# Kernel tuning notes

Hardware: AMD Instinct MI355X
Metric: run time of the kernel (lower is better)

## Reference

```python
import jax, jax.numpy as jnp
import numpy as np

N = 100000
E = 1600000
F_IN = 512
S_IN = 6
H = 64
C = 7


def gcn_conv(x, W, b, row, col, n):
    # PyG GCNConv: linear (no bias in lin), add self-loops, sym-normalize, scatter-add, + bias
    x = x @ W  # [N, out]
    loop = jnp.arange(n)
    r = jnp.concatenate([row, loop])
    c = jnp.concatenate([col, loop])
    deg = jax.ops.segment_sum(jnp.ones(r.shape, x.dtype), c, num_segments=n)
    dinv = jnp.where(deg > 0, deg ** -0.5, 0.0)
    norm = dinv[r] * dinv[c]  # [E+N]
    out = jax.ops.segment_sum(x[r] * norm[:, None], c, num_segments=n)
    return out + b


def setup_inputs() -> dict:
    key = jax.random.key(0)
    ks = jax.random.split(key, 12)
    feature = jax.random.normal(ks[0], (N, F_IN), jnp.float32)
    structure = jax.random.normal(ks[1], (N, S_IN), jnp.float32)
    edge_index = jax.random.randint(ks[2], (2, E), 0, N, dtype=jnp.int64)
    # glorot-ish param init
    def w(k, fan_in, fan_out):
        return jax.random.normal(k, (fan_in, fan_out), jnp.float32) * (1.0 / np.sqrt(fan_in))
    return {
        "feature": feature,
        "structure": structure,
        "edge_index": edge_index,
        "W_f": w(ks[3], F_IN, H), "b_f": jnp.zeros((H,), jnp.float32),
        "W_s": w(ks[4], S_IN, H), "b_s": jnp.zeros((H,), jnp.float32),
        "W_r": w(ks[5], 2 * H, C), "b_r": jnp.zeros((C,), jnp.float32),
        "emb": jax.random.normal(ks[6], (6, H), jnp.float32),
        "embW": jax.random.normal(ks[7], (H, 1), jnp.float32),
        "alpha_s": jnp.asarray(0.4, jnp.float32),
        "alpha_a": jnp.asarray(0.6, jnp.float32),
    }


def reference(feature, structure, edge_index, W_f, b_f, W_s, b_s, W_r, b_r, emb, embW, alpha_s, alpha_a):
    row, col = edge_index[0], edge_index[1]
    # branch 1: feature GCN (dropout is identity in eval mode)
    h_f = gcn_conv(feature, W_f, b_f, row, col, N)
    attr = h_f
    # embedding gate: sigmoid(emb @ embW) thresholded at 0.5 -> {0,1}
    gate = jax.nn.sigmoid(emb @ embW)  # [6,1]
    gate = jnp.where(gate < 0.5, 0.0, 1.0).astype(feature.dtype)
    struct_in = structure * gate[:, 0][None, :]  # [N,6] * [1,6]
    # branch 2: structure GCN
    h_s = gcn_conv(struct_in, W_s, b_s, row, col, N)
    struc = h_s
    # L1-normalize alphas (0.4,0.6 already sum to 1; torch does it via .data)
    denom = jax.lax.stop_gradient(jnp.abs(alpha_s) + jnp.abs(alpha_a))
    a_s = alpha_s / denom
    a_a = alpha_a / denom
    x = jnp.concatenate([attr * a_a * 2.0, struc * a_s * 2.0], axis=1)  # [N, 2H]
    y = gcn_conv(x, W_r, b_r, row, col, N)
    return (h_f, h_s, y)
```

## Files before the change

### kernel.cpp

```cpp
#include <hip/hip_runtime.h>
#include <hip/hip_bf16.h>


typedef __attribute__((ext_vector_type(8))) short bf16x8;
typedef __attribute__((ext_vector_type(4))) float f32x4;

__device__ __forceinline__ unsigned short f2bf(float x) {
    union { __hip_bfloat16 b; unsigned short u; } cv;
    cv.b = __float2bfloat16(x);
    return cv.u;
}
__device__ __forceinline__ float bf2f(unsigned short u) {
    union { unsigned u32; float f; } cv;
    cv.u32 = ((unsigned)u) << 16;
    return cv.f;
}

__global__ __launch_bounds__(256) void setup_prep_k(const float* __restrict__ emb,
                                                    const float* __restrict__ embW,
                                                    const float* __restrict__ alpha_s,
                                                    const float* __restrict__ alpha_a,
                                                    float* __restrict__ cw,
                                                    const float* __restrict__ Wf,
                                                    unsigned short* __restrict__ WthG,
                                                    unsigned short* __restrict__ WtlG,
                                                    unsigned* __restrict__ deg, int n) {
    if (blockIdx.x == 0) {
        if (threadIdx.x >= 64) return;
        int lane = threadIdx.x;
        float w = embW[lane];
        #pragma unroll
        for (int k = 0; k < 6; k++) {
            float p = emb[k * 64 + lane] * w;
            #pragma unroll
            for (int off = 32; off; off >>= 1) p += __shfl_xor(p, off);
            if (lane == 0) cw[k] = (p < 0.0f) ? 0.0f : 1.0f;
        }
        if (lane == 0) {
            float s = alpha_s[0];
            float a = alpha_a[0];
            float inv = 1.0f / (fabsf(s) + fabsf(a));
            cw[6] = 2.0f * a * inv;
            cw[7] = 2.0f * s * inv;
        }
        return;
    }
    if (blockIdx.x <= 128) {
        int idx = (blockIdx.x - 1) * 256 + threadIdx.x;
        int k = idx >> 6, c = idx & 63;
        float w = Wf[idx];
        unsigned short h = f2bf(w);
        unsigned short l = f2bf(w - bf2f(h));
        WthG[c * 512 + k] = h;
        WtlG[c * 512 + k] = l;
        return;
    }
    int start = (blockIdx.x - 129) * 1024 + threadIdx.x;
    #pragma unroll
    for (int k = 0; k < 4; k++) {
        int w = start + k * 256;
        if (w < n) deg[w] = 0u;
    }
}

__device__ __forceinline__ bool detect32(const int* p32, int e, int E, int lane) {
    int se = (e < E) ? e : lane;
    return __any(p32[2 * se + 1] != 0);
}

#define CHUNK 4096
__global__ __launch_bounds__(256) void degfill_k(const void* __restrict__ ei,
                                                 unsigned* __restrict__ deg,
                                                 int* __restrict__ slot, int E, int n) {
    int range = blockIdx.x & 7;
    int nper = (n + 7) >> 3;
    int lo = range * nper;
    int hi = min(n, lo + nper);
    int e0 = (blockIdx.x >> 3) * CHUNK + threadIdx.x;
    int lane = threadIdx.x & 63;
    const int* p32 = (const int*)ei;
    bool is32 = detect32(p32, e0, E, lane);

    int cs[16];
    #pragma unroll
    for (int k = 0; k < 16; k++) {
        int e = e0 + k * 256;
        cs[k] = -1;
        if (e < E)
            cs[k] = is32 ? p32[E + e] : (int)((const long long*)ei)[(size_t)E + e];
    }
    #pragma unroll
    for (int k = 0; k < 16; k++) {
        int c = cs[k];
        if (c < lo || c >= hi) continue;
        int e = e0 + k * 256;
        int r = is32 ? p32[e] : (int)((const long long*)ei)[(size_t)e];
        unsigned pos = atomicAdd(&deg[c], 1u);
        if (pos < 64u) slot[((size_t)c << 6) + pos] = r;
    }
}

__global__ void dinv_ss6_k(const unsigned* __restrict__ deg, float* __restrict__ dinv,
                           const float* __restrict__ structure, const float* __restrict__ cw,
                           unsigned short* __restrict__ ss6, int n) {
    int i = blockIdx.x * 256 + threadIdx.x;
    if (i >= n) return;
    float dv = rsqrtf((float)deg[i] + 1.0f);
    dinv[i] = dv;
    #pragma unroll
    for (int k = 0; k < 6; k++) ss6[i * 8 + k] = f2bf(structure[i * 6 + k] * cw[k] * dv);
    ss6[i * 8 + 6] = 0;
    ss6[i * 8 + 7] = 0;
}

__global__ __launch_bounds__(256) void gemm_f_mfma(const float* __restrict__ feat,
                                                   const unsigned short* __restrict__ WthG,
                                                   const unsigned short* __restrict__ WtlG,
                                                   const float* __restrict__ dinv,
                                                   unsigned short* __restrict__ xs, int n) {
    __shared__ unsigned short Ah[128 * 64];
    __shared__ unsigned short Bh[64 * 64];
    __shared__ unsigned short Bl[64 * 64];

    const int tid = threadIdx.x;
    const int blk = blockIdx.x;
    const int w = tid >> 6, l = tid & 63;
    const int lr = l & 15, lg = l >> 4;

    f32x4 acc[2][4];
    #pragma unroll
    for (int m = 0; m < 2; m++)
        #pragma unroll
        for (int nt = 0; nt < 4; nt++) acc[m][nt] = (f32x4)(0.0f);

    const int sr = tid >> 1, shalf = tid & 1;
    const int swc = tid >> 2, swq = tid & 3;
    const int gr_ld = min(blk * 128 + sr, n - 1);
    const float* asrc = feat + (size_t)gr_ld * 512 + shalf * 32;

    for (int k0 = 0; k0 < 512; k0 += 64) {
        {
            const float4* s4 = (const float4*)(asrc + k0);
            int base = sr * 128 + shalf * 64;
            int sw = (sr & 7) << 4;
            #pragma unroll
            for (int g = 0; g < 8; g++) {
                float4 v = s4[g];
                ushort4 h;
                h.x = f2bf(v.x); h.y = f2bf(v.y); h.z = f2bf(v.z); h.w = f2bf(v.w);
                *(ushort4*)((char*)Ah + ((base + g * 8) ^ sw)) = h;
            }
        }
        {
            int sw = (swc & 7) << 4;
            const unsigned short* wh = WthG + swc * 512 + k0;
            const unsigned short* wl = WtlG + swc * 512 + k0;
            #pragma unroll
            for (int s = 0; s < 2; s++) {
                int ko16 = swq * 2 + s;
                uint4 vh = *(const uint4*)(wh + ko16 * 8);
                uint4 vl = *(const uint4*)(wl + ko16 * 8);
                int off = (swc * 128 + ko16 * 16) ^ sw;
                *(uint4*)((char*)Bh + off) = vh;
                *(uint4*)((char*)Bl + off) = vl;
            }
        }
        __syncthreads();
        int swl = (lr & 7) << 4;
        #pragma unroll
        for (int ks = 0; ks < 2; ks++) {
            int koff = ks * 64 + lg * 16;
            int ra = ((w * 32 + lr) * 128 + koff) ^ swl;
            bf16x8 ah0 = *(const bf16x8*)((const char*)Ah + ra);
            bf16x8 ah1 = *(const bf16x8*)((const char*)Ah + ra + 16 * 128);
            #pragma unroll
            for (int nt = 0; nt < 4; nt++) {
                int cb = ((nt * 16 + lr) * 128 + koff) ^ swl;
                bf16x8 bh = *(const bf16x8*)((const char*)Bh + cb);
                bf16x8 bl = *(const bf16x8*)((const char*)Bl + cb);
                acc[0][nt] = __builtin_amdgcn_mfma_f32_16x16x32_bf16(ah0, bh, acc[0][nt], 0, 0, 0);
                acc[0][nt] = __builtin_amdgcn_mfma_f32_16x16x32_bf16(ah0, bl, acc[0][nt], 0, 0, 0);
                acc[1][nt] = __builtin_amdgcn_mfma_f32_16x16x32_bf16(ah1, bh, acc[1][nt], 0, 0, 0);
                acc[1][nt] = __builtin_amdgcn_mfma_f32_16x16x32_bf16(ah1, bl, acc[1][nt], 0, 0, 0);
            }
        }
        __syncthreads();
    }
    #pragma unroll
    for (int m = 0; m < 2; m++) {
        int row0 = blk * 128 + w * 32 + m * 16 + lg * 4;
        #pragma unroll
        for (int reg = 0; reg < 4; reg++) {
            int gr = row0 + reg;
            if (gr < n) {
                float dv = dinv[gr];
                #pragma unroll
                for (int nt = 0; nt < 4; nt++)
                    xs[(size_t)gr * 64 + nt * 16 + lr] = f2bf(acc[m][nt][reg] * dv);
            }
        }
    }
}

#define GATHER8(rl, g, accv, a6v)                                              \
    {                                                                          \
        int r0 = __shfl(rl, g + 0), r1 = __shfl(rl, g + 1);                    \
        int r2 = __shfl(rl, g + 2), r3 = __shfl(rl, g + 3);                    \
        int r4 = __shfl(rl, g + 4), r5 = __shfl(rl, g + 5);                    \
        int r6 = __shfl(rl, g + 6), r7 = __shfl(rl, g + 7);                    \
        float v0 = bf2f(xs[(size_t)r0 * 64 + lane]);                           \
        float v1 = bf2f(xs[(size_t)r1 * 64 + lane]);                           \
        float v2 = bf2f(xs[(size_t)r2 * 64 + lane]);                           \
        float v3 = bf2f(xs[(size_t)r3 * 64 + lane]);                           \
        float v4 = bf2f(xs[(size_t)r4 * 64 + lane]);                           \
        float v5 = bf2f(xs[(size_t)r5 * 64 + lane]);                           \
        float v6 = bf2f(xs[(size_t)r6 * 64 + lane]);                           \
        float v7 = bf2f(xs[(size_t)r7 * 64 + lane]);                           \
        accv += ((v0 + v1) + (v2 + v3)) + ((v4 + v5) + (v6 + v7));             \
        if (lane < 6) {                                                        \
            float u0 = bf2f(ss6[r0 * 8 + lane]), u1 = bf2f(ss6[r1 * 8 + lane]);\
            float u2 = bf2f(ss6[r2 * 8 + lane]), u3 = bf2f(ss6[r3 * 8 + lane]);\
            float u4 = bf2f(ss6[r4 * 8 + lane]), u5 = bf2f(ss6[r5 * 8 + lane]);\
            float u6 = bf2f(ss6[r6 * 8 + lane]), u7 = bf2f(ss6[r7 * 8 + lane]);\
            a6v += ((u0 + u1) + (u2 + u3)) + ((u4 + u5) + (u6 + u7));          \
        }                                                                      \
    }

__global__ __launch_bounds__(256) void agg_fs_k(const unsigned short* __restrict__ xs,
                                                const unsigned short* __restrict__ ss6,
                                                const int* __restrict__ slot,
                                                const unsigned* __restrict__ deg,
                                                const float* __restrict__ dinv,
                                                const float* __restrict__ cw,
                                                const float* __restrict__ bfv,
                                                const float* __restrict__ Ws,
                                                const float* __restrict__ bs,
                                                const float* __restrict__ Wr,
                                                float* __restrict__ out_hf,
                                                float* __restrict__ out_hs,
                                                unsigned short* __restrict__ ps, int n) {
    int wid = threadIdx.x >> 6;
    int lane = threadIdx.x & 63;
    int iA = blockIdx.x * 8 + wid * 2;
    int iB = iA + 1;
    if (iA >= n) return;
    bool hasB = iB < n;

    int dA = (int)min(deg[iA], 64u);
    int dB = hasB ? (int)min(deg[iB], 64u) : 0;

    float accA = bf2f(xs[(size_t)iA * 64 + lane]);
    float accB = hasB ? bf2f(xs[(size_t)iB * 64 + lane]) : 0.0f;
    float a6A = (lane < 6) ? bf2f(ss6[iA * 8 + lane]) : 0.0f;
    float a6B = (hasB && lane < 6) ? bf2f(ss6[iB * 8 + lane]) : 0.0f;

    int rlA = (lane < dA) ? slot[((size_t)iA << 6) + lane] : 0;
    int rlB = (lane < dB) ? slot[((size_t)iB << 6) + lane] : 0;
    int gmax = max(dA, dB);
    for (int g = 0; g + 8 <= gmax; g += 8) {
        if (g + 8 <= dA) GATHER8(rlA, g, accA, a6A);
        if (g + 8 <= dB) GATHER8(rlB, g, accB, a6B);
    }
    for (int d = dA & ~7; d < dA; d++) {
        int r = __shfl(rlA, d);
        accA += bf2f(xs[(size_t)r * 64 + lane]);
        if (lane < 6) a6A += bf2f(ss6[r * 8 + lane]);
    }
    for (int d = dB & ~7; d < dB; d++) {
        int r = __shfl(rlB, d);
        accB += bf2f(xs[(size_t)r * 64 + lane]);
        if (lane < 6) a6B += bf2f(ss6[r * 8 + lane]);
    }

    #pragma unroll
    for (int node = 0; node < 2; node++) {
        if (node == 1 && !hasB) break;
        int i = node ? iB : iA;
        float acc = node ? accB : accA;
        float a6 = node ? a6B : a6A;
        float di = dinv[i];
        float hf = acc * di + bfv[lane];
        float hs = bs[lane];
        #pragma unroll
        for (int k = 0; k < 6; k++) hs += __shfl(a6, k) * di * Ws[k * 64 + lane];
        out_hf[(size_t)i * 64 + lane] = hf;
        out_hs[(size_t)i * 64 + lane] = hs;

        float fa = hf * cw[6];
        float sa = hs * cw[7];
        #pragma unroll
        for (int j = 0; j < 7; j++) {
            float v = fa * Wr[lane * 7 + j] + sa * Wr[(64 + lane) * 7 + j];
            #pragma unroll
            for (int off = 32; off; off >>= 1) v += __shfl_xor(v, off);
            if (lane == j) ps[(size_t)i * 8 + j] = f2bf(v * di);
        }
        if (lane == 7) ps[(size_t)i * 8 + 7] = 0;
    }
}

__global__ __launch_bounds__(256) void agg_y_k(const unsigned short* __restrict__ ps,
                                               const int* __restrict__ slot,
                                               const unsigned* __restrict__ deg,
                                               const float* __restrict__ dinv,
                                               const float* __restrict__ br,
                                               float* __restrict__ out_y, int n) {
    int i = blockIdx.x * 4 + (threadIdx.x >> 6);
    int lane = threadIdx.x & 63;
    if (i >= n) return;
    int es = lane >> 3, j = lane & 7;
    int cnt = (int)min(deg[i], 64u);
    const int* srow = slot + ((size_t)i << 6);
    float acc = (es == 0) ? bf2f(ps[(size_t)i * 8 + j]) : 0.0f;
    int base = 0;
    for (; base + 16 <= cnt; base += 16) {
        int ra = srow[base + es];
        int rb = srow[base + 8 + es];
        acc += bf2f(ps[(size_t)ra * 8 + j]) + bf2f(ps[(size_t)rb * 8 + j]);
    }
    for (; base < cnt; base += 8) {
        int idx = base + es;
        if (idx < cnt) acc += bf2f(ps[(size_t)srow[idx] * 8 + j]);
    }
    acc += __shfl_xor(acc, 8);
    acc += __shfl_xor(acc, 16);
    acc += __shfl_xor(acc, 32);
    if (j < 7) out_y[(size_t)i * 7 + j] = acc * dinv[i] + br[j];
}

extern "C" void kernel_launch(void* const* d_in, const int* in_sizes, int n_in,
                              void* d_out, int out_size, void* d_ws, size_t ws_size,
                              hipStream_t stream) {
    const float* feature   = (const float*)d_in[0];
    const float* structure = (const float*)d_in[1];
    const void*  ei        = d_in[2];
    const float* Wf  = (const float*)d_in[3];
    const float* bfv = (const float*)d_in[4];
    const float* Ws  = (const float*)d_in[5];
    const float* bs  = (const float*)d_in[6];
    const float* Wr  = (const float*)d_in[7];
    const float* br  = (const float*)d_in[8];
    const float* emb = (const float*)d_in[9];
    const float* embW = (const float*)d_in[10];
    const float* alpha_s = (const float*)d_in[11];
    const float* alpha_a = (const float*)d_in[12];

    const int N = in_sizes[0] / 512;
    const int E = in_sizes[2] / 2;
    const int NB = (N + 255) / 256;
    const int NZ = (N + 1023) / 1024;
    const int NCH = (E + CHUNK - 1) / CHUNK;

    float* ws = (float*)d_ws;
    size_t XS     = 0;
    size_t SS6    = XS + (size_t)N * 32;
    size_t PS     = SS6 + (size_t)N * 4;
    size_t DINV   = PS + (size_t)N * 4;
    size_t DEG    = DINV + N;
    size_t CW     = DEG + N;
    size_t WT     = CW + 16;
    size_t SLOT   = WT + 32768;

    unsigned short* xs = (unsigned short*)(ws + XS);
    unsigned short* ss6 = (unsigned short*)(ws + SS6);
    unsigned short* ps = (unsigned short*)(ws + PS);
    float* dinv = ws + DINV;
    unsigned* deg = (unsigned*)(ws + DEG);
    float* cw = ws + CW;
    unsigned short* WthG = (unsigned short*)(ws + WT);
    unsigned short* WtlG = WthG + 512 * 64;
    int* slot = (int*)(ws + SLOT);

    setup_prep_k<<<129 + NZ, 256, 0, stream>>>(emb, embW, alpha_s, alpha_a, cw,
                                               Wf, WthG, WtlG, deg, N);
    degfill_k<<<NCH * 8, 256, 0, stream>>>(ei, deg, slot, E, N);
    dinv_ss6_k<<<NB, 256, 0, stream>>>(deg, dinv, structure, cw, ss6, N);
    gemm_f_mfma<<<(N + 127) / 128, 256, 0, stream>>>(feature, WthG, WtlG, dinv, xs, N);

    float* out_hf = (float*)d_out;
    float* out_hs = out_hf + (size_t)N * 64;
    float* out_y  = out_hf + (size_t)N * 128;
    agg_fs_k<<<(N + 7) / 8, 256, 0, stream>>>(xs, ss6, slot, deg, dinv, cw,
                                              bfv, Ws, bs, Wr, out_hf, out_hs, ps, N);
    agg_y_k<<<(N + 3) / 4, 256, 0, stream>>>(ps, slot, deg, dinv, br, out_y, N);
}
```

Before: 281.8 us.

## Load GEMM operands directly from global into registers, drop LDS staging

```diff
diff --git a/kernel.cpp b/kernel.cpp
--- a/kernel.cpp
+++ b/kernel.cpp
@@ -14,6 +14,14 @@
     union { unsigned u32; float f; } cv;
     cv.u32 = ((unsigned)u) << 16;
     return cv.f;
+}
+__device__ __forceinline__ bf16x8 cvt8(float4 a, float4 b) {
+    bf16x8 r;
+    r[0] = (short)f2bf(a.x); r[1] = (short)f2bf(a.y);
+    r[2] = (short)f2bf(a.z); r[3] = (short)f2bf(a.w);
+    r[4] = (short)f2bf(b.x); r[5] = (short)f2bf(b.y);
+    r[6] = (short)f2bf(b.z); r[7] = (short)f2bf(b.w);
+    return r;
 }
 
 __global__ __launch_bounds__(256) void setup_prep_k(const float* __restrict__ emb,
@@ -118,14 +126,17 @@
                                                    const unsigned short* __restrict__ WtlG,
                                                    const float* __restrict__ dinv,
                                                    unsigned short* __restrict__ xs, int n) {
-    __shared__ unsigned short Ah[128 * 64];
-    __shared__ unsigned short Bh[64 * 64];
-    __shared__ unsigned short Bl[64 * 64];
-
     const int tid = threadIdx.x;
-    const int blk = blockIdx.x;
     const int w = tid >> 6, l = tid & 63;
     const int lr = l & 15, lg = l >> 4;
+    const int rowbase = blockIdx.x * 128 + w * 32;
+    if (rowbase >= n + 31) {  }
+    const int r0 = min(rowbase + lr, n - 1);
+    const int r1 = min(rowbase + 16 + lr, n - 1);
+    const float* a0p = feat + (size_t)r0 * 512 + lg * 8;
+    const float* a1p = feat + (size_t)r1 * 512 + lg * 8;
+    const unsigned short* bhp = WthG + (size_t)lr * 512 + lg * 8;
+    const unsigned short* blp = WtlG + (size_t)lr * 512 + lg * 8;
 
     f32x4 acc[2][4];
     #pragma unroll
@@ -133,62 +144,38 @@
         #pragma unroll
         for (int nt = 0; nt < 4; nt++) acc[m][nt] = (f32x4)(0.0f);
 
-    const int sr = tid >> 1, shalf = tid & 1;
-    const int swc = tid >> 2, swq = tid & 3;
-    const int gr_ld = min(blk * 128 + sr, n - 1);
-    const float* asrc = feat + (size_t)gr_ld * 512 + shalf * 32;
-
-    for (int k0 = 0; k0 < 512; k0 += 64) {
-        {
-            const float4* s4 = (const float4*)(asrc + k0);
-            int base = sr * 128 + shalf * 64;
-            int sw = (sr & 7) << 4;
-            #pragma unroll
-            for (int g = 0; g < 8; g++) {
-                float4 v = s4[g];
-                ushort4 h;
-                h.x = f2bf(v.x); h.y = f2bf(v.y); h.z = f2bf(v.z); h.w = f2bf(v.w);
-                *(ushort4*)((char*)Ah + ((base + g * 8) ^ sw)) = h;
-            }
-        }
-        {
-            int sw = (swc & 7) << 4;
-            const unsigned short* wh = WthG + swc * 512 + k0;
-            const unsigned short* wl = WtlG + swc * 512 + k0;
-            #pragma unroll
-            for (int s = 0; s < 2; s++) {
-                int ko16 = swq * 2 + s;
-                uint4 vh = *(const uint4*)(wh + ko16 * 8);
-                uint4 vl = *(const uint4*)(wl + ko16 * 8);
-                int off = (swc * 128 + ko16 * 16) ^ sw;
-                *(uint4*)((char*)Bh + off) = vh;
-                *(uint4*)((char*)Bl + off) = vl;
-            }
-        }
-        __syncthreads();
-        int swl = (lr & 7) << 4;
-        #pragma unroll
-        for (int ks = 0; ks < 2; ks++) {
-            int koff = ks * 64 + lg * 16;
-            int ra = ((w * 32 + lr) * 128 + koff) ^ swl;
-            bf16x8 ah0 = *(const bf16x8*)((const char*)Ah + ra);
-            bf16x8 ah1 = *(const bf16x8*)((const char*)Ah + ra + 16 * 128);
-            #pragma unroll
-            for (int nt = 0; nt < 4; nt++) {
-                int cb = ((nt * 16 + lr) * 128 + koff) ^ swl;
-                bf16x8 bh = *(const bf16x8*)((const char*)Bh + cb);
-                bf16x8 bl = *(const bf16x8*)((const char*)Bl + cb);
-                acc[0][nt] = __builtin_amdgcn_mfma_f32_16x16x32_bf16(ah0, bh, acc[0][nt], 0, 0, 0);
-                acc[0][nt] = __builtin_amdgcn_mfma_f32_16x16x32_bf16(ah0, bl, acc[0][nt], 0, 0, 0);
-                acc[1][nt] = __builtin_amdgcn_mfma_f32_16x16x32_bf16(ah1, bh, acc[1][nt], 0, 0, 0);
-                acc[1][nt] = __builtin_amdgcn_mfma_f32_16x16x32_bf16(ah1, bl, acc[1][nt], 0, 0, 0);
-            }
-        }
-        __syncthreads();
+    float4 abuf[2][4];
+    abuf[0][0] = *(const float4*)(a0p);
+    abuf[0][1] = *(const float4*)(a0p + 4);
+    abuf[0][2] = *(const float4*)(a1p);
+    abuf[0][3] = *(const float4*)(a1p + 4);
+
+    #pragma unroll
+    for (int t = 0; t < 16; t++) {
+        const int cur = t & 1, nxt = cur ^ 1;
+        if (t + 1 < 16) {
+            int ko = (t + 1) * 32;
+            abuf[nxt][0] = *(const float4*)(a0p + ko);
+            abuf[nxt][1] = *(const float4*)(a0p + ko + 4);
+            abuf[nxt][2] = *(const float4*)(a1p + ko);
+            abuf[nxt][3] = *(const float4*)(a1p + ko + 4);
+        }
+        bf16x8 a0 = cvt8(abuf[cur][0], abuf[cur][1]);
+        bf16x8 a1 = cvt8(abuf[cur][2], abuf[cur][3]);
+        const int ko = t * 32;
+        #pragma unroll
+        for (int nt = 0; nt < 4; nt++) {
+            bf16x8 bh = *(const bf16x8*)(bhp + (size_t)nt * 16 * 512 + ko);
+            bf16x8 bl = *(const bf16x8*)(blp + (size_t)nt * 16 * 512 + ko);
+            acc[0][nt] = __builtin_amdgcn_mfma_f32_16x16x32_bf16(a0, bh, acc[0][nt], 0, 0, 0);
+            acc[0][nt] = __builtin_amdgcn_mfma_f32_16x16x32_bf16(a0, bl, acc[0][nt], 0, 0, 0);
+            acc[1][nt] = __builtin_amdgcn_mfma_f32_16x16x32_bf16(a1, bh, acc[1][nt], 0, 0, 0);
+            acc[1][nt] = __builtin_amdgcn_mfma_f32_16x16x32_bf16(a1, bl, acc[1][nt], 0, 0, 0);
+        }
     }
     #pragma unroll
     for (int m = 0; m < 2; m++) {
-        int row0 = blk * 128 + w * 32 + m * 16 + lg * 4;
+        int row0 = rowbase + m * 16 + lg * 4;
         #pragma unroll
         for (int reg = 0; reg < 4; reg++) {
             int gr = row0 + reg;
```

Result: slower. 315.9 us (+12.1%).
